# Performance work log

Measured on AMD Instinct MI355X. Metric: run time of the kernel, lower is better.

The kernel has to match this reference:

```python
import jax, jax.numpy as jnp
import numpy as np

N_EMBED = 1024
N_HEADS = 16
HEAD_DIM = N_EMBED // N_HEADS


def setup_inputs() -> dict:
    key = jax.random.key(0)
    ks = jax.random.split(key, 5)
    x = jax.random.normal(ks[0], (4, 2048, N_EMBED), dtype=jnp.float32)
    # Linear params stored as [in, out] (y = x @ W + b), math-equivalent to torch Linear
    scale_attn = 1.0 / np.sqrt(N_EMBED)
    W_attn = jax.random.normal(ks[1], (N_EMBED, 3 * N_EMBED), dtype=jnp.float32) * scale_attn
    b_attn = jax.random.normal(ks[2], (3 * N_EMBED,), dtype=jnp.float32) * 0.02
    W_proj = jax.random.normal(ks[3], (N_EMBED, N_EMBED), dtype=jnp.float32) * scale_attn
    b_proj = jax.random.normal(ks[4], (N_EMBED,), dtype=jnp.float32) * 0.02
    return {"x": x, "W_attn": W_attn, "b_attn": b_attn, "W_proj": W_proj, "b_proj": b_proj}


def reference(x, W_attn, b_attn, W_proj, b_proj):
    BS, SL, ED = x.shape
    qkv = x @ W_attn + b_attn                      # [B, S, 3E]
    q, k, v = jnp.split(qkv, 3, axis=2)
    # [B, H, S, D]
    def heads(t):
        return t.reshape(BS, SL, N_HEADS, HEAD_DIM).transpose(0, 2, 1, 3)
    q, k, v = heads(q), heads(k), heads(v)
    att = jnp.einsum('bhqd,bhkd->bhqk', q, k) * (HEAD_DIM ** -0.5)
    causal = jnp.tril(jnp.ones((SL, SL), dtype=bool))
    att = jnp.where(causal[None, None], att, -jnp.inf)
    att = jax.nn.softmax(att, axis=-1)
    y = jnp.einsum('bhqk,bhkd->bhqd', att, v)      # [B, H, S, D]
    y = y.transpose(0, 2, 1, 3).reshape(BS, SL, ED)
    return y @ W_proj + b_proj
```

## Files before the change

### kernel.cpp

```cpp
#include <hip/hip_runtime.h>


#define BATCH 4
#define SEQ   2048
#define EMB   1024
#define NH    16
#define HD    64

typedef __bf16 bf16;
typedef __bf16 bf16x8 __attribute__((ext_vector_type(8)));
typedef float  f32x4  __attribute__((ext_vector_type(4)));

__device__ __forceinline__ void ld_lds16(const void* g, void* l) {
  __builtin_amdgcn_global_load_lds(
      (const __attribute__((address_space(1))) void*)g,
      (__attribute__((address_space(3))) void*)l, 16, 0, 0);
}

__global__ void cvt_f32_bf16(const float* __restrict__ in, bf16* __restrict__ out, int n) {
  int i = (blockIdx.x * blockDim.x + threadIdx.x) * 4;
  if (i + 3 < n) {
    float4 v = *(const float4*)(in + i);
    bf16 o0 = (bf16)v.x, o1 = (bf16)v.y, o2 = (bf16)v.z, o3 = (bf16)v.w;
    out[i] = o0; out[i+1] = o1; out[i+2] = o2; out[i+3] = o3;
  }
}

__global__ void transpose_cvt2(const float* __restrict__ Wa, const float* __restrict__ Wp,
                               bf16* __restrict__ WaT, bf16* __restrict__ WpT) {
  __shared__ float tile[32][33];
  int bx = blockIdx.x;
  const float* W; bf16* WT; int N;
  if (bx < 96) { W = Wa; WT = WaT; N = 3072; }
  else         { W = Wp; WT = WpT; N = 1024; bx -= 96; }
  int n0 = bx * 32, k0 = blockIdx.y * 32;
  int tx = threadIdx.x & 31, ty = threadIdx.x >> 5;
#pragma unroll
  for (int r = 0; r < 4; r++) {
    int k = k0 + ty + r * 8;
    tile[ty + r * 8][tx] = W[(long)k * N + n0 + tx];
  }
  __syncthreads();
#pragma unroll
  for (int r = 0; r < 4; r++) {
    int n = n0 + ty + r * 8;
    WT[(long)n * EMB + k0 + tx] = (bf16)tile[tx][ty + r * 8];
  }
}

#define QSCALE 0.18033688f

template <int MODE, int NF>
__global__ __launch_bounds__(512, 2) void gemm8p(
    const bf16* __restrict__ A, const bf16* __restrict__ Bt,
    const float* __restrict__ bias,
    bf16* __restrict__ q, bf16* __restrict__ k, bf16* __restrict__ v,
    float* __restrict__ out)
{
  constexpr int BN = NF * 64;
  constexpr int WN = NF * 16;
  constexpr int BELEM = BN * 32;
  __shared__ __align__(16) bf16 lds[16384 + 2 * BELEM];
  int lin = blockIdx.x;
  int xcd = lin & 7, s = lin >> 3;
  int by = xcd * 4 + (s & 3);
  int bx = s >> 2;
  int m0 = by * 256, n0 = bx * BN;
  int t = threadIdx.x;
  int wid = t >> 6, lane = t & 63;
  int l15 = lane & 15, quad = lane >> 4;
  int wr = wid >> 2, wc = wid & 3;

  const bf16* Ag = A + (long)m0 * EMB;
  const bf16* Bg = Bt + (long)n0 * EMB;

  f32x4 acc[8][NF] = {};
  bf16x8 af[8], bfr[NF];
  constexpr int NT = EMB / 32;

#define LDSA(b) (lds + (b) * 8192)
#define LDSB(b) (lds + 16384 + (b) * BELEM)

#define ISSUE128(gbase, rowoff, ldst, ktt)                                     \
  { int r_ = (rowoff) + (t >> 2);                                              \
    ld_lds16(&(gbase)[(long)r_ * EMB + (ktt) + (((t & 3) ^ (r_ & 3)) * 8)],    \
             (ldst) + ((rowoff) + wid * 16) * 32); }

#define RD_A(mi) { int r_ = wr * 128 + (mi) * 16 + l15;                        \
    af[mi] = *(const bf16x8*)&Ab[r_ * 32 + ((quad ^ (r_ & 3)) * 8)]; }
#define RD_B(ni) { int r_ = wc * WN + (ni) * 16 + l15;                         \
    bfr[ni] = *(const bf16x8*)&Bb[r_ * 32 + ((quad ^ (r_ & 3)) * 8)]; }

#define FENCE asm volatile("" ::: "memory")
#define BAR   { FENCE; __builtin_amdgcn_s_barrier(); FENCE; }

#define MFMAC(nlo)                                                             \
  { __builtin_amdgcn_s_setprio(1);                                             \
    _Pragma("unroll") for (int mi_ = 0; mi_ < 8; ++mi_)                        \
      _Pragma("unroll") for (int nj_ = 0; nj_ < NF / 2; ++nj_)                 \
        acc[mi_][(nlo) + nj_] = __builtin_amdgcn_mfma_f32_16x16x32_bf16(       \
            af[mi_], bfr[(nlo) + nj_], acc[mi_][(nlo) + nj_], 0, 0, 0);        \
    __builtin_amdgcn_s_setprio(0); }

  ISSUE128(Ag, 0,   LDSA(0), 0);
  ISSUE128(Ag, 128, LDSA(0), 0);
  ISSUE128(Bg, 0,   LDSB(0), 0);
  if constexpr (NF == 4) ISSUE128(Bg, 128, LDSB(0), 0);
  ISSUE128(Ag, 0,   LDSA(1), 32);
  asm volatile("s_waitcnt vmcnt(1)" ::: "memory");
  BAR;

#pragma unroll 2
  for (int tt = 0; tt < NT; ++tt) {
    const bf16* Ab = LDSA(tt & 1);
    const bf16* Bb = LDSB(tt & 1);
    bf16* An = LDSA((tt + 1) & 1);
    bf16* Bn = LDSB((tt + 1) & 1);
    bf16* Ac = LDSA(tt & 1);
    int kn  = (tt + 1 < NT ? tt + 1 : NT - 1) * 32;
    int kn2 = (tt + 2 < NT ? tt + 2 : NT - 1) * 32;

#pragma unroll
    for (int mi = 0; mi < 8; ++mi) RD_A(mi);
#pragma unroll
    for (int ni = 0; ni < NF / 2; ++ni) RD_B(ni);
    ISSUE128(Ag, 128, An, kn);
    ISSUE128(Bg, 0,   Bn, kn);
    if constexpr (NF == 4) ISSUE128(Bg, 128, Bn, kn);
    BAR; MFMAC(0); BAR;
#pragma unroll
    for (int ni = NF / 2; ni < NF; ++ni) RD_B(ni);
    ISSUE128(Ag, 0, Ac, kn2);
    asm volatile("s_waitcnt vmcnt(1)" ::: "memory");
    BAR; MFMAC(NF / 2); BAR;
  }

  asm volatile("s_waitcnt vmcnt(0)" ::: "memory");
  __syncthreads();

  if (MODE == 1) {
#pragma unroll
    for (int mi = 0; mi < 8; ++mi)
#pragma unroll
      for (int ni = 0; ni < NF; ++ni) {
        int gcol = n0 + wc * WN + ni * 16 + l15;
        float bv = bias[gcol];
#pragma unroll
        for (int i = 0; i < 4; ++i) {
          int grow = m0 + wr * 128 + mi * 16 + quad * 4 + i;
          out[(long)grow * EMB + gcol] = acc[mi][ni][i] + bv;
        }
      }
  } else {
    int which = n0 >> 10;
    if (which < 2) {
      bf16* dst = (which == 0) ? q : k;
      float scale = (which == 0) ? QSCALE : 1.0f;
#pragma unroll
      for (int mi = 0; mi < 8; ++mi)
#pragma unroll
        for (int ni = 0; ni < NF; ++ni) {
          int gcol = n0 + wc * WN + ni * 16 + l15;
          float bv = bias[gcol];
          int e = gcol & 1023, h = e >> 6, d = e & 63;
#pragma unroll
          for (int i = 0; i < 4; ++i) {
            int grow = m0 + wr * 128 + mi * 16 + quad * 4 + i;
            int b = grow >> 11, ss = grow & 2047;
            dst[(((long)b * NH + h) * SEQ + ss) * HD + d] =
                (bf16)((acc[mi][ni][i] + bv) * scale);
          }
        }
    } else {
#pragma unroll
      for (int mi = 0; mi < 8; ++mi)
#pragma unroll
        for (int ni = 0; ni < NF; ++ni) {
          int gcol = n0 + wc * WN + ni * 16 + l15;
          float bv = bias[gcol];
          int e = gcol & 1023, h = e >> 6, d = e & 63;
#pragma unroll
          for (int i = 0; i < 4; ++i) {
            int grow = m0 + wr * 128 + mi * 16 + quad * 4 + i;
            int b = grow >> 11, ss = grow & 2047;
            v[(((long)b * NH + h) * HD + d) * SEQ + ss] =
                (bf16)(acc[mi][ni][i] + bv);
          }
        }
    }
  }
#undef LDSA
#undef LDSB
#undef ISSUE128
#undef RD_A
#undef RD_B
#undef MFMAC
}

#define LDP 72

__global__ __launch_bounds__(256, 2) void attn(
    const bf16* __restrict__ Q, const bf16* __restrict__ K,
    const bf16* __restrict__ Vt, bf16* __restrict__ Y)
{
  __shared__ __align__(16) bf16 Kl[64 * 64];
  __shared__ __align__(16) bf16 Vl[64 * 64];
  __shared__ __align__(16) bf16 Pl[4][32 * LDP];
  int L = blockIdx.x;
  int a = L >> 3;
  int hd = (L & 7) + 8 * (a & 7);
  int st = a >> 3;
  int b = hd >> 4, h = hd & 15;
  const bf16* Qp  = Q  + (((long)b * NH + h) * SEQ) * HD;
  const bf16* Kp  = K  + (((long)b * NH + h) * SEQ) * HD;
  const bf16* Vtp = Vt + (((long)b * NH + h) * HD) * SEQ;
  int t = threadIdx.x, wave = t >> 6, lane = t & 63;
  int l15 = lane & 15, quad = lane >> 4;

#pragma unroll 1
  for (int pass = 0; pass < 2; ++pass) {
    int q0 = (pass == 0) ? st * 128 : (SEQ - 128) - st * 128;
    int wq0 = q0 + wave * 32;

    bf16x8 qf[2][2];
#pragma unroll
    for (int m = 0; m < 2; ++m) {
      const bf16* qrow = Qp + (long)(wq0 + m * 16 + l15) * HD + quad * 8;
      qf[m][0] = *(const bf16x8*)(qrow);
      qf[m][1] = *(const bf16x8*)(qrow + 32);
    }
    float lrow[2][4] = {};
    f32x4 oacc[2][4] = {};

    int ntiles = q0 / 64 + 2;
#pragma unroll 1
    for (int kt = 0; kt < ntiles; ++kt) {
      int k0 = kt * 64;
      __syncthreads();
#pragma unroll
      for (int it = 0; it < 2; ++it) {
        int cu = it * 256 + t;
        int row = cu >> 3, u = cu & 7;
        ld_lds16(&Kp[(long)(k0 + row) * HD + ((u ^ (row & 7)) * 8)],
                 &Kl[(it * 256 + wave * 64) * 8]);
        ld_lds16(&Vtp[(long)row * SEQ + k0 + ((u ^ (row & 7)) * 8)],
                 &Vl[(it * 256 + wave * 64) * 8]);
      }
      __syncthreads();
      if (k0 > wq0 + 31) continue;

      f32x4 sc[2][4] = {};
#pragma unroll
      for (int kk = 0; kk < 2; ++kk) {
#pragma unroll
        for (int ni = 0; ni < 4; ++ni) {
          int r = ni * 16 + l15, u = kk * 4 + quad;
          bf16x8 kfr = *(const bf16x8*)(&Kl[r * 64 + ((u ^ (r & 7)) * 8)]);
          sc[0][ni] = __builtin_amdgcn_mfma_f32_16x16x32_bf16(qf[0][kk], kfr, sc[0][ni], 0, 0, 0);
          sc[1][ni] = __builtin_amdgcn_mfma_f32_16x16x32_bf16(qf[1][kk], kfr, sc[1][ni], 0, 0, 0);
        }
      }

      bool full = (k0 + 63 <= wq0);
#pragma unroll
      for (int m = 0; m < 2; ++m) {
#pragma unroll
        for (int i = 0; i < 4; ++i) {
          int qr = wq0 + m * 16 + quad * 4 + i;
          float e[4];
#pragma unroll
          for (int ni = 0; ni < 4; ++ni) {
            float x = sc[m][ni][i];
            if (!full) x = (k0 + ni * 16 + l15 <= qr) ? x : -1e30f;
            e[ni] = __builtin_amdgcn_exp2f(x);
          }
          lrow[m][i] += (e[0] + e[1]) + (e[2] + e[3]);
          int prow = (m * 16 + quad * 4 + i) * LDP;
#pragma unroll
          for (int ni = 0; ni < 4; ++ni)
            Pl[wave][prow + ni * 16 + l15] = (bf16)e[ni];
        }
      }
      asm volatile("s_waitcnt lgkmcnt(0)" ::: "memory");
#pragma unroll
      for (int kk = 0; kk < 2; ++kk) {
        int kbase = kk * 32 + quad * 8;
        bf16x8 pf0 = *(const bf16x8*)(&Pl[wave][(l15) * LDP + kbase]);
        bf16x8 pf1 = *(const bf16x8*)(&Pl[wave][(16 + l15) * LDP + kbase]);
#pragma unroll
        for (int ni = 0; ni < 4; ++ni) {
          int dd = ni * 16 + l15, u = kk * 4 + quad;
          bf16x8 vf = *(const bf16x8*)(&Vl[dd * 64 + ((u ^ (dd & 7)) * 8)]);
          oacc[0][ni] = __builtin_amdgcn_mfma_f32_16x16x32_bf16(pf0, vf, oacc[0][ni], 0, 0, 0);
          oacc[1][ni] = __builtin_amdgcn_mfma_f32_16x16x32_bf16(pf1, vf, oacc[1][ni], 0, 0, 0);
        }
      }
    }
#pragma unroll
    for (int m = 0; m < 2; ++m) {
#pragma unroll
      for (int i = 0; i < 4; ++i) {
        float rs = lrow[m][i];
#pragma unroll
        for (int off = 8; off; off >>= 1) rs += __shfl_xor(rs, off, 16);
        float inv = 1.0f / rs;
        int qr = wq0 + m * 16 + quad * 4 + i;
        bf16* dst = Y + ((long)(b * SEQ + qr)) * EMB + h * HD;
#pragma unroll
        for (int ni = 0; ni < 4; ++ni)
          dst[ni * 16 + l15] = (bf16)(oacc[m][ni][i] * inv);
      }
    }
  }
}

extern "C" void kernel_launch(void* const* d_in, const int* in_sizes, int n_in,
                              void* d_out, int out_size, void* d_ws, size_t ws_size,
                              hipStream_t stream) {
  const float* x      = (const float*)d_in[0];
  const float* W_attn = (const float*)d_in[1];
  const float* b_attn = (const float*)d_in[2];
  const float* W_proj = (const float*)d_in[3];
  const float* b_proj = (const float*)d_in[4];
  float* out = (float*)d_out;
  char* ws = (char*)d_ws;
  bf16* xb  = (bf16*)(ws);
  bf16* WaT = (bf16*)(ws + 16777216);
  bf16* WpT = (bf16*)(ws + 23068672);
  bf16* Qb  = (bf16*)(ws + 25165824);
  bf16* Kb  = (bf16*)(ws + 41943040);
  bf16* Vtb = (bf16*)(ws + 58720256);
  bf16* Yb  = (bf16*)(ws + 75497472);

  cvt_f32_bf16<<<8192, 256, 0, stream>>>(x, xb, BATCH * SEQ * EMB);
  transpose_cvt2<<<dim3(128, 32), 256, 0, stream>>>(W_attn, W_proj, WaT, WpT);
  gemm8p<0, 4><<<384, 512, 0, stream>>>(xb, WaT, b_attn, Qb, Kb, Vtb, nullptr);
  attn<<<512, 256, 0, stream>>>(Qb, Kb, Vtb, Yb);
  gemm8p<1, 2><<<256, 512, 0, stream>>>(Yb, WpT, b_proj,
                                        nullptr, nullptr, nullptr, out);
}
```

Measured before the change: 271.3 us.

## Add dedicated smaller-tile projection GEMM and change QKV LDS swizzle pattern

Replaces the templated 256x128-tile GEMM for the output projection with a new 128x64-tile kernel over 1024 blocks of 256 threads. The aim is better CU occupancy and load balance on the smaller projection GEMM. The QKV GEMM is de-templated and its LDS swizzle changes from XOR to an add/subtract rotation, meant to reduce bank conflicts. In exchange, the new proj kernel has no double buffering, so load latency is less hidden, and the new swizzle's correctness depends on the store and read mappings matching.

Measured after the change: 256.3 us. -5.5%, faster.

```diff
diff --git a/kernel.cpp b/kernel.cpp
--- a/kernel.cpp
+++ b/kernel.cpp
@@ -50,22 +50,17 @@
 
 #define QSCALE 0.18033688f
 
-template <int MODE, int NF>
 __global__ __launch_bounds__(512, 2) void gemm8p(
     const bf16* __restrict__ A, const bf16* __restrict__ Bt,
     const float* __restrict__ bias,
-    bf16* __restrict__ q, bf16* __restrict__ k, bf16* __restrict__ v,
-    float* __restrict__ out)
+    bf16* __restrict__ q, bf16* __restrict__ k, bf16* __restrict__ v)
 {
-  constexpr int BN = NF * 64;
-  constexpr int WN = NF * 16;
-  constexpr int BELEM = BN * 32;
-  __shared__ __align__(16) bf16 lds[16384 + 2 * BELEM];
+  __shared__ __align__(16) bf16 lds[3 * 16384];
   int lin = blockIdx.x;
   int xcd = lin & 7, s = lin >> 3;
   int by = xcd * 4 + (s & 3);
   int bx = s >> 2;
-  int m0 = by * 256, n0 = bx * BN;
+  int m0 = by * 256, n0 = bx * 256;
   int t = threadIdx.x;
   int wid = t >> 6, lane = t & 63;
   int l15 = lane & 15, quad = lane >> 4;
@@ -74,22 +69,24 @@
   const bf16* Ag = A + (long)m0 * EMB;
   const bf16* Bg = Bt + (long)n0 * EMB;
 
-  f32x4 acc[8][NF] = {};
-  bf16x8 af[8], bfr[NF];
+  f32x4 acc[8][4] = {};
+  bf16x8 af[8], bfr[4];
   constexpr int NT = EMB / 32;
+  int ph8 = ((quad + (l15 >> 1)) & 3) * 8;
 
 #define LDSA(b) (lds + (b) * 8192)
-#define LDSB(b) (lds + 16384 + (b) * BELEM)
+#define LDSB(b) (lds + 16384 + (b) * 8192)
 
 #define ISSUE128(gbase, rowoff, ldst, ktt)                                     \
   { int r_ = (rowoff) + (t >> 2);                                              \
-    ld_lds16(&(gbase)[(long)r_ * EMB + (ktt) + (((t & 3) ^ (r_ & 3)) * 8)],    \
+    int g_ = ((t & 3) - ((t >> 3) & 3)) & 3;                                   \
+    ld_lds16(&(gbase)[(long)r_ * EMB + (ktt) + g_ * 8],                        \
              (ldst) + ((rowoff) + wid * 16) * 32); }
 
 #define RD_A(mi) { int r_ = wr * 128 + (mi) * 16 + l15;                        \
-    af[mi] = *(const bf16x8*)&Ab[r_ * 32 + ((quad ^ (r_ & 3)) * 8)]; }
-#define RD_B(ni) { int r_ = wc * WN + (ni) * 16 + l15;                         \
-    bfr[ni] = *(const bf16x8*)&Bb[r_ * 32 + ((quad ^ (r_ & 3)) * 8)]; }
+    af[mi] = *(const bf16x8*)&Ab[r_ * 32 + ph8]; }
+#define RD_B(ni) { int r_ = wc * 64 + (ni) * 16 + l15;                         \
+    bfr[ni] = *(const bf16x8*)&Bb[r_ * 32 + ph8]; }
 
 #define FENCE asm volatile("" ::: "memory")
 #define BAR   { FENCE; __builtin_amdgcn_s_barrier(); FENCE; }
@@ -97,7 +94,7 @@
 #define MFMAC(nlo)                                                             \
   { __builtin_amdgcn_s_setprio(1);                                             \
     _Pragma("unroll") for (int mi_ = 0; mi_ < 8; ++mi_)                        \
-      _Pragma("unroll") for (int nj_ = 0; nj_ < NF / 2; ++nj_)                 \
+      _Pragma("unroll") for (int nj_ = 0; nj_ < 2; ++nj_)                      \
         acc[mi_][(nlo) + nj_] = __builtin_amdgcn_mfma_f32_16x16x32_bf16(       \
             af[mi_], bfr[(nlo) + nj_], acc[mi_][(nlo) + nj_], 0, 0, 0);        \
     __builtin_amdgcn_s_setprio(0); }
@@ -105,7 +102,7 @@
   ISSUE128(Ag, 0,   LDSA(0), 0);
   ISSUE128(Ag, 128, LDSA(0), 0);
   ISSUE128(Bg, 0,   LDSB(0), 0);
-  if constexpr (NF == 4) ISSUE128(Bg, 128, LDSB(0), 0);
+  ISSUE128(Bg, 128, LDSB(0), 0);
   ISSUE128(Ag, 0,   LDSA(1), 32);
   asm volatile("s_waitcnt vmcnt(1)" ::: "memory");
   BAR;
@@ -122,72 +119,55 @@
 
 #pragma unroll
     for (int mi = 0; mi < 8; ++mi) RD_A(mi);
-#pragma unroll
-    for (int ni = 0; ni < NF / 2; ++ni) RD_B(ni);
+    RD_B(0); RD_B(1);
     ISSUE128(Ag, 128, An, kn);
     ISSUE128(Bg, 0,   Bn, kn);
-    if constexpr (NF == 4) ISSUE128(Bg, 128, Bn, kn);
+    ISSUE128(Bg, 128, Bn, kn);
     BAR; MFMAC(0); BAR;
-#pragma unroll
-    for (int ni = NF / 2; ni < NF; ++ni) RD_B(ni);
+    RD_B(2); RD_B(3);
     ISSUE128(Ag, 0, Ac, kn2);
     asm volatile("s_waitcnt vmcnt(1)" ::: "memory");
-    BAR; MFMAC(NF / 2); BAR;
+    BAR; MFMAC(2); BAR;
   }
 
   asm volatile("s_waitcnt vmcnt(0)" ::: "memory");
   __syncthreads();
 
-  if (MODE == 1) {
+  int which = n0 >> 10;
+  if (which < 2) {
+    bf16* dst = (which == 0) ? q : k;
+    float scale = (which == 0) ? QSCALE : 1.0f;
 #pragma unroll
     for (int mi = 0; mi < 8; ++mi)
 #pragma unroll
-      for (int ni = 0; ni < NF; ++ni) {
-        int gcol = n0 + wc * WN + ni * 16 + l15;
+      for (int ni = 0; ni < 4; ++ni) {
+        int gcol = n0 + wc * 64 + ni * 16 + l15;
         float bv = bias[gcol];
+        int e = gcol & 1023, h = e >> 6, d = e & 63;
 #pragma unroll
         for (int i = 0; i < 4; ++i) {
           int grow = m0 + wr * 128 + mi * 16 + quad * 4 + i;
-          out[(long)grow * EMB + gcol] = acc[mi][ni][i] + bv;
+          int b = grow >> 11, ss = grow & 2047;
+          dst[(((long)b * NH + h) * SEQ + ss) * HD + d] =
+              (bf16)((acc[mi][ni][i] + bv) * scale);
         }
       }
   } else {
-    int which = n0 >> 10;
-    if (which < 2) {
-      bf16* dst = (which == 0) ? q : k;
-      float scale = (which == 0) ? QSCALE : 1.0f;
-#pragma unroll
-      for (int mi = 0; mi < 8; ++mi)
-#pragma unroll
-        for (int ni = 0; ni < NF; ++ni) {
-          int gcol = n0 + wc * WN + ni * 16 + l15;
-          float bv = bias[gcol];
-          int e = gcol & 1023, h = e >> 6, d = e & 63;
-#pragma unroll
-          for (int i = 0; i < 4; ++i) {
-            int grow = m0 + wr * 128 + mi * 16 + quad * 4 + i;
-            int b = grow >> 11, ss = grow & 2047;
-            dst[(((long)b * NH + h) * SEQ + ss) * HD + d] =
-                (bf16)((acc[mi][ni][i] + bv) * scale);
-          }
-        }
-    } else {
-#pragma unroll
-      for (int mi = 0; mi < 8; ++mi)
-#pragma unroll
-        for (int ni = 0; ni < NF; ++ni) {
-          int gcol = n0 + wc * WN + ni * 16 + l15;
-          float bv = bias[gcol];
-          int e = gcol & 1023, h = e >> 6, d = e & 63;
-#pragma unroll
-          for (int i = 0; i < 4; ++i) {
-            int grow = m0 + wr * 128 + mi * 16 + quad * 4 + i;
-            int b = grow >> 11, ss = grow & 2047;
-            v[(((long)b * NH + h) * HD + d) * SEQ + ss] =
-                (bf16)(acc[mi][ni][i] + bv);
-          }
-        }
-    }
+#pragma unroll
+    for (int mi = 0; mi < 8; ++mi)
+#pragma unroll
+      for (int ni = 0; ni < 4; ++ni) {
+        int gcol = n0 + wc * 64 + ni * 16 + l15;
+        float bv = bias[gcol];
+        int e = gcol & 1023, h = e >> 6, d = e & 63;
+#pragma unroll
+        for (int i = 0; i < 4; ++i) {
+          int grow = m0 + wr * 128 + mi * 16 + quad * 4 + i;
+          int b = grow >> 11, ss = grow & 2047;
+          v[(((long)b * NH + h) * HD + d) * SEQ + ss] =
+              (bf16)(acc[mi][ni][i] + bv);
+        }
+      }
   }
 #undef LDSA
 #undef LDSB
@@ -195,6 +175,79 @@
 #undef RD_A
 #undef RD_B
 #undef MFMAC
+}
+
+__global__ __launch_bounds__(256, 3) void gemm_proj(
+    const bf16* __restrict__ A, const bf16* __restrict__ Bt,
+    const float* __restrict__ bias, float* __restrict__ out)
+{
+  __shared__ __align__(16) bf16 Al[128 * 64];
+  __shared__ __align__(16) bf16 Bl[64 * 64];
+  int lin = blockIdx.x;
+  int xcd = lin & 7, s = lin >> 3;
+  int bx = s >> 3, by = xcd * 8 + (s & 7);
+  int m0 = by * 128;
+  int n0 = bx * 64;
+  int t = threadIdx.x;
+  int wave = t >> 6, lane = t & 63;
+  int l15 = lane & 15, quad = lane >> 4;
+  int wm = (wave & 1) * 64, wn = (wave >> 1) * 32;
+
+  f32x4 acc[4][2] = {};
+
+  for (int kt = 0; kt < EMB; kt += 64) {
+    __syncthreads();
+#pragma unroll
+    for (int it = 0; it < 4; ++it) {
+      int c = it * 256 + t;
+      int row = c >> 3, u = c & 7;
+      ld_lds16(&A[(long)(m0 + row) * EMB + kt + ((u ^ (row & 7)) * 8)],
+               &Al[(it * 256 + wave * 64) * 8]);
+    }
+    {
+      int c = t;
+      int row = c >> 3, u = c & 7;
+      ld_lds16(&Bt[(long)(n0 + row) * EMB + kt + ((u ^ (row & 7)) * 8)],
+               &Bl[(wave * 64) * 8]);
+      c = 256 + t;
+      row = c >> 3; u = c & 7;
+      ld_lds16(&Bt[(long)(n0 + row) * EMB + kt + ((u ^ (row & 7)) * 8)],
+               &Bl[(256 + wave * 64) * 8]);
+    }
+    __syncthreads();
+#pragma unroll
+    for (int ks = 0; ks < 2; ++ks) {
+      bf16x8 af[4], bfr[2];
+#pragma unroll
+      for (int i = 0; i < 4; ++i) {
+        int r = wm + i * 16 + l15;
+        af[i] = *(const bf16x8*)(&Al[r * 64 + (((ks * 4 + quad) ^ (r & 7)) * 8)]);
+      }
+#pragma unroll
+      for (int i = 0; i < 2; ++i) {
+        int r = wn + i * 16 + l15;
+        bfr[i] = *(const bf16x8*)(&Bl[r * 64 + (((ks * 4 + quad) ^ (r & 7)) * 8)]);
+      }
+#pragma unroll
+      for (int mi = 0; mi < 4; ++mi)
+#pragma unroll
+        for (int ni = 0; ni < 2; ++ni)
+          acc[mi][ni] = __builtin_amdgcn_mfma_f32_16x16x32_bf16(af[mi], bfr[ni], acc[mi][ni], 0, 0, 0);
+    }
+  }
+
+#pragma unroll
+  for (int mi = 0; mi < 4; ++mi)
+#pragma unroll
+    for (int ni = 0; ni < 2; ++ni) {
+      int gcol = n0 + wn + ni * 16 + l15;
+      float bv = bias[gcol];
+#pragma unroll
+      for (int i = 0; i < 4; ++i) {
+        int grow = m0 + wm + mi * 16 + quad * 4 + i;
+        out[(long)grow * EMB + gcol] = acc[mi][ni][i] + bv;
+      }
+    }
 }
 
 #define LDP 72
@@ -334,8 +387,7 @@
 
   cvt_f32_bf16<<<8192, 256, 0, stream>>>(x, xb, BATCH * SEQ * EMB);
   transpose_cvt2<<<dim3(128, 32), 256, 0, stream>>>(W_attn, W_proj, WaT, WpT);
-  gemm8p<0, 4><<<384, 512, 0, stream>>>(xb, WaT, b_attn, Qb, Kb, Vtb, nullptr);
+  gemm8p<<<384, 512, 0, stream>>>(xb, WaT, b_attn, Qb, Kb, Vtb);
   attn<<<512, 256, 0, stream>>>(Qb, Kb, Vtb, Yb);
-  gemm8p<1, 2><<<256, 512, 0, stream>>>(Yb, WpT, b_proj,
-                                        nullptr, nullptr, nullptr, out);
-}
+  gemm_proj<<<1024, 256, 0, stream>>>(Yb, WpT, b_proj, out);
+}
```
